# Kernel tuning notes

Hardware: AMD Instinct MI355X
Metric: run time of the kernel (lower is better)

The kernel has to match this reference:

```python
import jax, jax.numpy as jnp
import numpy as np

B, N, E, DIN, DOUT = 2, 50000, 800000, 128, 128
ALPHA = 0.2  # LeakyReLU negative slope


def setup_inputs() -> dict:
    key = jax.random.key(0)
    k1, k2, k3, k4 = jax.random.split(key, 4)
    h = jax.random.normal(k1, (B, N, DIN), dtype=jnp.float32)
    edge_index = jax.random.randint(k4, (2, E), 0, N, dtype=jnp.int32)
    # Linear(in, out, bias=False): weight shape [out, in]
    W_fc = jax.random.normal(k2, (DOUT, DIN), dtype=jnp.float32) / np.sqrt(DIN)
    # Linear(2*out, 1, bias=False): weight shape [1, 2*out]
    W_attn = jax.random.normal(k3, (1, 2 * DOUT), dtype=jnp.float32) / np.sqrt(2 * DOUT)
    return {"h": h, "edge_index": edge_index, "W_fc": W_fc, "W_attn": W_attn}


def reference(h, edge_index, W_fc, W_attn):
    # Wh: [B, N, DOUT]
    Wh = jnp.einsum("bni,oi->bno", h, W_fc)
    src, dst = edge_index[0], edge_index[1]
    # attn_fc([src_h, dst_h]) == src_h @ a_src + dst_h @ a_dst
    a = W_attn[0]
    a_src, a_dst = a[:DOUT], a[DOUT:]
    s_src = Wh @ a_src  # [B, N]
    s_dst = Wh @ a_dst  # [B, N]
    e = jax.nn.leaky_relu(s_src[:, src] + s_dst[:, dst], ALPHA)  # [B, E]
    # segment softmax over destination groups (segment ops need leading E axis)
    eT = e.T  # [E, B]
    m = jax.ops.segment_max(eT, dst, num_segments=N)  # [N, B]; -inf for empty segs (never gathered)
    ex = jnp.exp(eT - m[dst])  # [E, B]
    denom = jax.ops.segment_sum(ex, dst, num_segments=N)  # [N, B]
    attn = ex / denom[dst]  # [E, B]
    # weighted scatter-add of source features: msg [E, B, DOUT]
    msg = attn[:, :, None] * jnp.transpose(Wh, (1, 0, 2))[src]
    out = jax.ops.segment_sum(msg, dst, num_segments=N)  # [N, B, DOUT]
    return jax.nn.elu(jnp.transpose(out, (1, 0, 2)))  # [B, N, DOUT]
```

## Files before the change

### kernel.cpp

```cpp
#include <hip/hip_runtime.h>
#include <math.h>

#define NN 50000
#define EE 800000
#define DDIM 128
#define NROWS 100000
#define NBIN 391
#define NCHUNK 391
#define GEMMB 1563

typedef __attribute__((ext_vector_type(8))) short bf16x8;
typedef __attribute__((ext_vector_type(4))) float f32x4;

__device__ __forceinline__ float lrelu(float x) { return x > 0.f ? x : 0.2f * x; }
__device__ __forceinline__ float eluf(float x)  {
    float e = __expf(x);
    return x > 0.f ? x : e - 1.f;
}

__device__ __forceinline__ unsigned short f2bf(float f) {
    unsigned int u = __float_as_uint(f);
    u += 0x7fffu + ((u >> 16) & 1u);
    return (unsigned short)(u >> 16);
}
__device__ __forceinline__ float bflo(unsigned int v) { return __uint_as_float(v << 16); }
__device__ __forceinline__ float bfhi(unsigned int v) { return __uint_as_float(v & 0xffff0000u); }

__global__ __launch_bounds__(256) void wprep_kernel(const float* __restrict__ Wfc,
                                                    unsigned short* __restrict__ Wsw) {
    const int tid = threadIdx.x;
    const int col = tid & 127;
    const int kh  = tid >> 7;
#pragma unroll
    for (int q8 = 0; q8 < 8; ++q8) {
        int k0 = kh * 64 + q8 * 8;
        float4 w0 = *(const float4*)&Wfc[col * DDIM + k0];
        float4 w1 = *(const float4*)&Wfc[col * DDIM + k0 + 4];
        union { uint4 q4; unsigned short u[8]; } pk;
        pk.u[0] = f2bf(w0.x); pk.u[1] = f2bf(w0.y);
        pk.u[2] = f2bf(w0.z); pk.u[3] = f2bf(w0.w);
        pk.u[4] = f2bf(w1.x); pk.u[5] = f2bf(w1.y);
        pk.u[6] = f2bf(w1.z); pk.u[7] = f2bf(w1.w);
        int chunk = (k0 >> 3) ^ (col & 15);
        *(uint4*)((char*)Wsw + col * 256 + chunk * 16) = pk.q4;
    }
}

__global__ __launch_bounds__(256) void fused_kernel(const int* __restrict__ ei,
                                                    int* __restrict__ histmat,
                                                    const float* __restrict__ h,
                                                    const unsigned short* __restrict__ Wsw,
                                                    const float* __restrict__ Wat,
                                                    unsigned short* __restrict__ Wh16,
                                                    float* __restrict__ ssrc,
                                                    float* __restrict__ sdst) {
    __shared__ unsigned int Wlds_u32[8192];
    __shared__ unsigned short stage[64 * 136];
    const int tid = threadIdx.x;

    if (blockIdx.x < NCHUNK) {
        int* lcnt = (int*)Wlds_u32;
        for (int i = tid; i < NBIN; i += 256) lcnt[i] = 0;
        __syncthreads();
        const int cb  = blockIdx.x * 2048;
        const int cnt = min(2048, EE - cb);
#pragma unroll
        for (int r = 0; r < 8; ++r) {
            int el = r * 256 + tid;
            if (el < cnt) atomicAdd(&lcnt[ei[EE + cb + el] >> 7], 1);
        }
        __syncthreads();
        for (int i = tid; i < NBIN; i += 256)
            histmat[blockIdx.x * NBIN + i] = lcnt[i];
        return;
    }

    char* WldsB  = (char*)Wlds_u32;
    char* stageB = (char*)stage;
    const int gb   = blockIdx.x - NCHUNK;
    const int lane = tid & 63;
    const int wv   = tid >> 6;

    {
        const char* gsrc = (const char*)Wsw + wv * 8192 + lane * 16;
        unsigned int* ldst = &Wlds_u32[wv * 2048];
#pragma unroll
        for (int c8 = 0; c8 < 8; ++c8) {
            __builtin_amdgcn_global_load_lds((const unsigned int*)(gsrc + c8 * 1024),
                                             ldst + c8 * 256, 16, 0, 0);
        }
    }

    const long mbase  = (long)gb * 64 + wv * 16;
    const bool active = (mbase < NROWS);
    const long mload  = active ? mbase : 0;
    const int c  = lane & 15;
    const int kg = lane >> 4;

    union Af { bf16x8 v; unsigned short u[8]; };
    Af af[4];
    const float* arow = h + (mload + c) * DDIM + kg * 8;
#pragma unroll
    for (int kk = 0; kk < 4; ++kk) {
        float4 x = *(const float4*)(arow + kk * 32);
        float4 y = *(const float4*)(arow + kk * 32 + 4);
        af[kk].u[0] = f2bf(x.x); af[kk].u[1] = f2bf(x.y);
        af[kk].u[2] = f2bf(x.z); af[kk].u[3] = f2bf(x.w);
        af[kk].u[4] = f2bf(y.x); af[kk].u[5] = f2bf(y.y);
        af[kk].u[6] = f2bf(y.z); af[kk].u[7] = f2bf(y.w);
    }
    __syncthreads();
    if (!active) return;

    f32x4 acc[8];
#pragma unroll
    for (int t = 0; t < 8; ++t) acc[t] = (f32x4){0.f, 0.f, 0.f, 0.f};
#pragma unroll
    for (int t = 0; t < 8; ++t) {
        int colbase = (t * 16 + c) * 256;
        int sw = c << 4;
#pragma unroll
        for (int kk = 0; kk < 4; ++kk) {
            int ba = (colbase + kk * 64 + kg * 16) ^ sw;
            bf16x8 b = *(const bf16x8*)(WldsB + ba);
            acc[t] = __builtin_amdgcn_mfma_f32_16x16x32_bf16(af[kk].v, b, acc[t], 0, 0, 0);
        }
    }

#pragma unroll
    for (int t = 0; t < 8; ++t) {
#pragma unroll
        for (int r = 0; r < 4; ++r) {
            int lrow = wv * 16 + kg * 4 + r;
            *(unsigned short*)(stageB + lrow * 272 + (t * 16 + c) * 2) = f2bf(acc[t][r]);
        }
    }
    {
        const long gbase = mbase * 256;
        const int  lbase = wv * 16 * 272;
#pragma unroll
        for (int q = 0; q < 4; ++q) {
            int f = q * 1024 + lane * 16;
            uint4 v = *(const uint4*)(stageB + lbase + (f >> 8) * 272 + (f & 255));
            *(uint4*)((char*)Wh16 + gbase + f) = v;
        }
    }

    float asv[8], adv[8];
#pragma unroll
    for (int t = 0; t < 8; ++t) {
        asv[t] = Wat[t * 16 + c];
        adv[t] = Wat[DDIM + t * 16 + c];
    }
#pragma unroll
    for (int r = 0; r < 4; ++r) {
        float ps = 0.f, pd = 0.f;
#pragma unroll
        for (int t = 0; t < 8; ++t) {
            ps += acc[t][r] * asv[t];
            pd += acc[t][r] * adv[t];
        }
#pragma unroll
        for (int o = 1; o <= 8; o <<= 1) {
            ps += __shfl_xor(ps, o);
            pd += __shfl_xor(pd, o);
        }
        if (c == 0) {
            long row = mbase + kg * 4 + r;
            ssrc[row] = ps;
            sdst[row] = pd;
        }
    }
}

__global__ __launch_bounds__(64) void colscan_kernel(const int* __restrict__ histmat,
                                                     int* __restrict__ chunkstart,
                                                     int* __restrict__ bintot) {
    const int bin  = blockIdx.x;
    const int lane = threadIdx.x;
    int carry = 0;
#pragma unroll
    for (int it = 0; it < 7; ++it) {
        int c = it * 64 + lane;
        int v = (c < NCHUNK) ? histmat[c * NBIN + bin] : 0;
        int x = v;
#pragma unroll
        for (int o = 1; o < 64; o <<= 1) {
            int t = __shfl_up(x, o);
            if (lane >= o) x += t;
        }
        if (c < NCHUNK) chunkstart[bin * NCHUNK + c] = carry + x - v;
        carry += __shfl(x, 63);
    }
    if (lane == 0) bintot[bin] = carry;
}

__global__ __launch_bounds__(64) void binscan_kernel(const int* __restrict__ bintot,
                                                     int* __restrict__ binbase) {
    const int lane = threadIdx.x;
    int carry = 0;
#pragma unroll
    for (int it = 0; it < 7; ++it) {
        int c = it * 64 + lane;
        int v = (c < NBIN) ? bintot[c] : 0;
        int x = v;
#pragma unroll
        for (int o = 1; o < 64; o <<= 1) {
            int t = __shfl_up(x, o);
            if (lane >= o) x += t;
        }
        if (c < NBIN) binbase[c] = carry + x - v;
        carry += __shfl(x, 63);
    }
    if (lane == 0) binbase[NBIN] = carry;
}

__global__ __launch_bounds__(256) void scatterA_kernel(const int* __restrict__ ei,
                                                       const int* __restrict__ binbase,
                                                       const int* __restrict__ chunkstart,
                                                       unsigned int* __restrict__ records) {
    __shared__ int lcnt[NBIN];
    __shared__ int lbase[NBIN];
    const int tid = threadIdx.x;
    for (int i = tid; i < NBIN; i += 256) {
        lcnt[i]  = 0;
        lbase[i] = binbase[i] + chunkstart[i * NCHUNK + blockIdx.x];
    }
    __syncthreads();
    const int cb  = blockIdx.x * 2048;
    const int cnt = min(2048, EE - cb);
#pragma unroll
    for (int r = 0; r < 8; ++r) {
        int el = r * 256 + tid;
        if (el < cnt) {
            int e   = cb + el;
            int dst = ei[EE + e];
            int src = ei[e];
            int bin = dst >> 7;
            int rank = atomicAdd(&lcnt[bin], 1);
            records[lbase[bin] + rank] = (unsigned)src | ((unsigned)(dst & 127) << 16);
        }
    }
}

__global__ __launch_bounds__(256) void scatterB_kernel(const unsigned int* __restrict__ records,
                                                       const int* __restrict__ binbase,
                                                       int* __restrict__ offs,
                                                       int* __restrict__ slist) {
    __shared__ int cnt[128];
    __shared__ int cbase[128];
    const int b = blockIdx.x, tid = threadIdx.x;
    const int start = binbase[b];
    const int end   = binbase[b + 1];
    const int span  = end - start;

    if (tid < 128) cnt[tid] = 0;
    __syncthreads();
    for (int i = tid; i < span; i += 256)
        atomicAdd(&cnt[records[start + i] >> 16], 1);
    __syncthreads();
    if (tid < 64) {
        int l = tid;
        int c0 = cnt[l], c1 = cnt[64 + l];
        int s0 = c0, s1 = c1;
#pragma unroll
        for (int o = 1; o < 64; o <<= 1) { int t = __shfl_up(s0, o); if (l >= o) s0 += t; }
        int t0 = __shfl(s0, 63);
#pragma unroll
        for (int o = 1; o < 64; o <<= 1) { int t = __shfl_up(s1, o); if (l >= o) s1 += t; }
        cbase[l]      = s0 - c0;
        cbase[64 + l] = t0 + s1 - c1;
    }
    __syncthreads();
    if (tid < 128) {
        offs[b * 128 + tid] = start + cbase[tid];
        cnt[tid] = 0;
    }
    __syncthreads();
    for (int i = tid; i < span; i += 256) {
        unsigned int r = records[start + i];
        int dl = (int)(r >> 16);
        int pos = atomicAdd(&cnt[dl], 1);
        slist[start + cbase[dl] + pos] = (int)(r & 0xFFFFu);
    }
}

__global__ __launch_bounds__(256) void aggregate_kernel(const unsigned int* __restrict__ Wh16u,
                                                        const int* __restrict__ offs,
                                                        const int* __restrict__ slist,
                                                        const float* __restrict__ ssrc,
                                                        const float* __restrict__ sdst,
                                                        float* __restrict__ out) {
    const int lane = threadIdx.x & 63;
    const int wid  = threadIdx.x >> 6;
    const int bid  = blockIdx.x;
    const int b    = bid & 1;
    const int d    = (bid >> 1) * 4 + wid;

    const int grp = lane >> 4;
    const int fl  = lane & 15;

    float* o = out + ((long)b * NN + d) * DDIM;

    const int base   = offs[d];
    const int degree = offs[d + 1] - base;
    if (degree == 0) {
        if (lane < 16) {
            float4 z = {0.f, 0.f, 0.f, 0.f};
            ((float4*)o)[2 * fl]     = z;
            ((float4*)o)[2 * fl + 1] = z;
        }
        return;
    }

    const long boff = (long)b * NN;
    const float sdv = sdst[boff + d];
    const float* ssb = ssrc + boff;
    const unsigned int* WB = Wh16u + boff * 64;

    f32x4 accA = {0,0,0,0}, accB = {0,0,0,0};
    float ds = 0.f;

    for (int ch = 0; ch < degree; ch += 64) {
        int i = ch + lane;
        int s = 0; float w = 0.f;
        if (i < degree) {
            s = slist[base + i];
            w = __expf(lrelu(ssb[s] + sdv));
            ds += w;
        }
        int cnt   = min(64, degree - ch);
        int quads = (cnt + 3) >> 2;
        for (int j = 0; j < quads; ++j) {
            int idx = 4 * j + grp;
            int   sj = __shfl(s, idx);
            float wj = __shfl(w, idx);
            uint4 v = ((const uint4*)(WB + (long)sj * 64))[fl];
            accA.x += wj * bflo(v.x); accA.y += wj * bfhi(v.x);
            accA.z += wj * bflo(v.y); accA.w += wj * bfhi(v.y);
            accB.x += wj * bflo(v.z); accB.y += wj * bfhi(v.z);
            accB.z += wj * bflo(v.w); accB.w += wj * bfhi(v.w);
        }
    }

#pragma unroll
    for (int m = 32; m >= 16; m >>= 1) {
        accA.x += __shfl_xor(accA.x, m); accA.y += __shfl_xor(accA.y, m);
        accA.z += __shfl_xor(accA.z, m); accA.w += __shfl_xor(accA.w, m);
        accB.x += __shfl_xor(accB.x, m); accB.y += __shfl_xor(accB.y, m);
        accB.z += __shfl_xor(accB.z, m); accB.w += __shfl_xor(accB.w, m);
    }
#pragma unroll
    for (int m = 32; m > 0; m >>= 1) ds += __shfl_xor(ds, m);
    const float inv = 1.f / ds;

    if (lane < 16) {
        float4 rA = { eluf(accA.x * inv), eluf(accA.y * inv),
                      eluf(accA.z * inv), eluf(accA.w * inv) };
        float4 rB = { eluf(accB.x * inv), eluf(accB.y * inv),
                      eluf(accB.z * inv), eluf(accB.w * inv) };
        ((float4*)o)[2 * fl]     = rA;
        ((float4*)o)[2 * fl + 1] = rB;
    }
}

extern "C" void kernel_launch(void* const* d_in, const int* in_sizes, int n_in,
                              void* d_out, int out_size, void* d_ws, size_t ws_size,
                              hipStream_t stream) {
    (void)in_sizes; (void)n_in; (void)out_size; (void)ws_size;
    const float* h   = (const float*)d_in[0];
    const int*   ei  = (const int*)d_in[1];
    const float* Wfc = (const float*)d_in[2];
    const float* Wat = (const float*)d_in[3];
    float* out = (float*)d_out;

    char* ws = (char*)d_ws;
    unsigned short* Wh16 = (unsigned short*)(ws + 0);
    float*  ssrc  = (float*)(ws + 25600000);
    float*  sdst  = (float*)(ws + 26000000);
    int*    slist = (int*)  (ws + 26400000);
    unsigned int* records = (unsigned int*)(ws + 29600000);
    int*    offs      = (int*)(ws + 32800000);
    int*    histmat   = (int*)(ws + 33000192);
    int*    chunkstart= (int*)(ws + 33611716);
    int*    bintot    = (int*)(ws + 34223240);
    int*    binbase   = (int*)(ws + 34224804);
    unsigned short* Wsw = (unsigned short*)(ws + 34226384);

    wprep_kernel<<<1, 256, 0, stream>>>(Wfc, Wsw);
    fused_kernel<<<NCHUNK + GEMMB, 256, 0, stream>>>(ei, histmat, h, Wsw, Wat,
                                                     Wh16, ssrc, sdst);
    colscan_kernel<<<NBIN, 64, 0, stream>>>(histmat, chunkstart, bintot);
    binscan_kernel<<<1, 64, 0, stream>>>(bintot, binbase);
    scatterA_kernel<<<NCHUNK, 256, 0, stream>>>(ei, binbase, chunkstart, records);
    scatterB_kernel<<<NBIN, 256, 0, stream>>>(records, binbase, offs, slist);
    aggregate_kernel<<<25000, 256, 0, stream>>>((const unsigned int*)Wh16, offs,
                                                slist, ssrc, sdst, out);
}
```

Before: 116.5 us.

## Regroup pipeline stages to cut launches and hide scatter under GEMM

The destination histogram moves into the weight-prep kernel, and the scatter-to-bins pass now runs in the same grid as the feature GEMM, so the two overlap. The separate bin-scan kernel is removed: each scatter block, and each scatterB block, recomputes the 391-entry exclusive scan of bin totals locally. The launch sequence drops from seven kernels to five. In exchange every block repeats a small scan, and the binbase buffer is gone.

```diff
diff --git a/kernel.cpp b/kernel.cpp
--- a/kernel.cpp
+++ b/kernel.cpp
@@ -26,9 +26,27 @@
 __device__ __forceinline__ float bflo(unsigned int v) { return __uint_as_float(v << 16); }
 __device__ __forceinline__ float bfhi(unsigned int v) { return __uint_as_float(v & 0xffff0000u); }
 
-__global__ __launch_bounds__(256) void wprep_kernel(const float* __restrict__ Wfc,
+__global__ __launch_bounds__(256) void histW_kernel(const int* __restrict__ ei,
+                                                    int* __restrict__ histmat,
+                                                    const float* __restrict__ Wfc,
                                                     unsigned short* __restrict__ Wsw) {
     const int tid = threadIdx.x;
+    if (blockIdx.x < NCHUNK) {
+        __shared__ int lcnt[NBIN];
+        for (int i = tid; i < NBIN; i += 256) lcnt[i] = 0;
+        __syncthreads();
+        const int cb  = blockIdx.x * 2048;
+        const int cnt = min(2048, EE - cb);
+#pragma unroll
+        for (int r = 0; r < 8; ++r) {
+            int el = r * 256 + tid;
+            if (el < cnt) atomicAdd(&lcnt[ei[EE + cb + el] >> 7], 1);
+        }
+        __syncthreads();
+        for (int i = tid; i < NBIN; i += 256)
+            histmat[blockIdx.x * NBIN + i] = lcnt[i];
+        return;
+    }
     const int col = tid & 127;
     const int kh  = tid >> 7;
 #pragma unroll
@@ -46,32 +64,82 @@
     }
 }
 
-__global__ __launch_bounds__(256) void fused_kernel(const int* __restrict__ ei,
-                                                    int* __restrict__ histmat,
-                                                    const float* __restrict__ h,
-                                                    const unsigned short* __restrict__ Wsw,
-                                                    const float* __restrict__ Wat,
-                                                    unsigned short* __restrict__ Wh16,
-                                                    float* __restrict__ ssrc,
-                                                    float* __restrict__ sdst) {
+__global__ __launch_bounds__(64) void colscan_kernel(const int* __restrict__ histmat,
+                                                     int* __restrict__ chunkstart,
+                                                     int* __restrict__ bintot) {
+    const int bin  = blockIdx.x;
+    const int lane = threadIdx.x;
+    int carry = 0;
+#pragma unroll
+    for (int it = 0; it < 7; ++it) {
+        int c = it * 64 + lane;
+        int v = (c < NCHUNK) ? histmat[c * NBIN + bin] : 0;
+        int x = v;
+#pragma unroll
+        for (int o = 1; o < 64; o <<= 1) {
+            int t = __shfl_up(x, o);
+            if (lane >= o) x += t;
+        }
+        if (c < NCHUNK) chunkstart[bin * NCHUNK + c] = carry + x - v;
+        carry += __shfl(x, 63);
+    }
+    if (lane == 0) bintot[bin] = carry;
+}
+
+__global__ __launch_bounds__(256) void fusedAG_kernel(const int* __restrict__ ei,
+                                                      const int* __restrict__ bintot,
+                                                      const int* __restrict__ chunkstart,
+                                                      unsigned int* __restrict__ records,
+                                                      const float* __restrict__ h,
+                                                      const unsigned short* __restrict__ Wsw,
+                                                      const float* __restrict__ Wat,
+                                                      unsigned short* __restrict__ Wh16,
+                                                      float* __restrict__ ssrc,
+                                                      float* __restrict__ sdst) {
     __shared__ unsigned int Wlds_u32[8192];
     __shared__ unsigned short stage[64 * 136];
     const int tid = threadIdx.x;
 
     if (blockIdx.x < NCHUNK) {
-        int* lcnt = (int*)Wlds_u32;
-        for (int i = tid; i < NBIN; i += 256) lcnt[i] = 0;
+        int* lcnt  = (int*)Wlds_u32;
+        int* lbase = (int*)Wlds_u32 + 512;
+        int* bb    = (int*)Wlds_u32 + 1024;
+        if (tid < 64) {
+            int carry = 0;
+#pragma unroll
+            for (int it = 0; it < 7; ++it) {
+                int c = it * 64 + tid;
+                int v = (c < NBIN) ? bintot[c] : 0;
+                int x = v;
+#pragma unroll
+                for (int o = 1; o < 64; o <<= 1) {
+                    int t = __shfl_up(x, o);
+                    if (tid >= o) x += t;
+                }
+                if (c < NBIN) bb[c] = carry + x - v;
+                carry += __shfl(x, 63);
+            }
+        }
+        __syncthreads();
+        for (int i = tid; i < NBIN; i += 256) {
+            lcnt[i]  = 0;
+            lbase[i] = bb[i] + chunkstart[i * NCHUNK + blockIdx.x];
+        }
         __syncthreads();
         const int cb  = blockIdx.x * 2048;
         const int cnt = min(2048, EE - cb);
 #pragma unroll
         for (int r = 0; r < 8; ++r) {
             int el = r * 256 + tid;
-            if (el < cnt) atomicAdd(&lcnt[ei[EE + cb + el] >> 7], 1);
-        }
-        __syncthreads();
-        for (int i = tid; i < NBIN; i += 256)
-            histmat[blockIdx.x * NBIN + i] = lcnt[i];
+            if (el < cnt) {
+                int e   = cb + el;
+                int dst = ei[EE + e];
+                int src = ei[e];
+                int bin = dst >> 7;
+                int rank = atomicAdd(&lcnt[bin], 1);
+                records[lbase[bin] + rank] = (unsigned)src | ((unsigned)(dst & 127) << 16);
+            }
+        }
         return;
     }
 
@@ -137,11 +205,11 @@
     }
     {
         const long gbase = mbase * 256;
-        const int  lbase = wv * 16 * 272;
+        const int  lbase2 = wv * 16 * 272;
 #pragma unroll
         for (int q = 0; q < 4; ++q) {
             int f = q * 1024 + lane * 16;
-            uint4 v = *(const uint4*)(stageB + lbase + (f >> 8) * 272 + (f & 255));
+            uint4 v = *(const uint4*)(stageB + lbase2 + (f >> 8) * 272 + (f & 255));
             *(uint4*)((char*)Wh16 + gbase + f) = v;
         }
     }
@@ -173,89 +241,38 @@
     }
 }
 
-__global__ __launch_bounds__(64) void colscan_kernel(const int* __restrict__ histmat,
-                                                     int* __restrict__ chunkstart,
-                                                     int* __restrict__ bintot) {
-    const int bin  = blockIdx.x;
-    const int lane = threadIdx.x;
-    int carry = 0;
-#pragma unroll
-    for (int it = 0; it < 7; ++it) {
-        int c = it * 64 + lane;
-        int v = (c < NCHUNK) ? histmat[c * NBIN + bin] : 0;
-        int x = v;
-#pragma unroll
-        for (int o = 1; o < 64; o <<= 1) {
-            int t = __shfl_up(x, o);
-            if (lane >= o) x += t;
-        }
-        if (c < NCHUNK) chunkstart[bin * NCHUNK + c] = carry + x - v;
-        carry += __shfl(x, 63);
-    }
-    if (lane == 0) bintot[bin] = carry;
-}
-
-__global__ __launch_bounds__(64) void binscan_kernel(const int* __restrict__ bintot,
-                                                     int* __restrict__ binbase) {
-    const int lane = threadIdx.x;
-    int carry = 0;
-#pragma unroll
-    for (int it = 0; it < 7; ++it) {
-        int c = it * 64 + lane;
-        int v = (c < NBIN) ? bintot[c] : 0;
-        int x = v;
-#pragma unroll
-        for (int o = 1; o < 64; o <<= 1) {
-            int t = __shfl_up(x, o);
-            if (lane >= o) x += t;
-        }
-        if (c < NBIN) binbase[c] = carry + x - v;
-        carry += __shfl(x, 63);
-    }
-    if (lane == 0) binbase[NBIN] = carry;
-}
-
-__global__ __launch_bounds__(256) void scatterA_kernel(const int* __restrict__ ei,
-                                                       const int* __restrict__ binbase,
-                                                       const int* __restrict__ chunkstart,
-                                                       unsigned int* __restrict__ records) {
-    __shared__ int lcnt[NBIN];
-    __shared__ int lbase[NBIN];
-    const int tid = threadIdx.x;
-    for (int i = tid; i < NBIN; i += 256) {
-        lcnt[i]  = 0;
-        lbase[i] = binbase[i] + chunkstart[i * NCHUNK + blockIdx.x];
-    }
-    __syncthreads();
-    const int cb  = blockIdx.x * 2048;
-    const int cnt = min(2048, EE - cb);
-#pragma unroll
-    for (int r = 0; r < 8; ++r) {
-        int el = r * 256 + tid;
-        if (el < cnt) {
-            int e   = cb + el;
-            int dst = ei[EE + e];
-            int src = ei[e];
-            int bin = dst >> 7;
-            int rank = atomicAdd(&lcnt[bin], 1);
-            records[lbase[bin] + rank] = (unsigned)src | ((unsigned)(dst & 127) << 16);
-        }
-    }
-}
-
 __global__ __launch_bounds__(256) void scatterB_kernel(const unsigned int* __restrict__ records,
-                                                       const int* __restrict__ binbase,
+                                                       const int* __restrict__ bintot,
                                                        int* __restrict__ offs,
                                                        int* __restrict__ slist) {
     __shared__ int cnt[128];
     __shared__ int cbase[128];
+    __shared__ int bb2[2];
     const int b = blockIdx.x, tid = threadIdx.x;
-    const int start = binbase[b];
-    const int end   = binbase[b + 1];
-    const int span  = end - start;
-
+
+    if (tid < 64) {
+        int carry = 0;
+#pragma unroll
+        for (int it = 0; it < 7; ++it) {
+            int c = it * 64 + tid;
+            int v = (c < NBIN) ? bintot[c] : 0;
+            int x = v;
+#pragma unroll
+            for (int o = 1; o < 64; o <<= 1) {
+                int t = __shfl_up(x, o);
+                if (tid >= o) x += t;
+            }
+            int excl = carry + x - v;
+            if (c == b)     bb2[0] = excl;
+            if (c == b + 1) bb2[1] = excl;
+            carry += __shfl(x, 63);
+        }
+    }
     if (tid < 128) cnt[tid] = 0;
     __syncthreads();
+    const int start = bb2[0];
+    const int span  = bb2[1] - start;
+
     for (int i = tid; i < span; i += 256)
         atomicAdd(&cnt[records[start + i] >> 16], 1);
     __syncthreads();
@@ -384,16 +401,13 @@
     int*    histmat   = (int*)(ws + 33000192);
     int*    chunkstart= (int*)(ws + 33611716);
     int*    bintot    = (int*)(ws + 34223240);
-    int*    binbase   = (int*)(ws + 34224804);
-    unsigned short* Wsw = (unsigned short*)(ws + 34226384);
-
-    wprep_kernel<<<1, 256, 0, stream>>>(Wfc, Wsw);
-    fused_kernel<<<NCHUNK + GEMMB, 256, 0, stream>>>(ei, histmat, h, Wsw, Wat,
-                                                     Wh16, ssrc, sdst);
+    unsigned short* Wsw = (unsigned short*)(ws + 34224816);
+
+    histW_kernel<<<NCHUNK + 1, 256, 0, stream>>>(ei, histmat, Wfc, Wsw);
     colscan_kernel<<<NBIN, 64, 0, stream>>>(histmat, chunkstart, bintot);
-    binscan_kernel<<<1, 64, 0, stream>>>(bintot, binbase);
-    scatterA_kernel<<<NCHUNK, 256, 0, stream>>>(ei, binbase, chunkstart, records);
-    scatterB_kernel<<<NBIN, 256, 0, stream>>>(records, binbase, offs, slist);
+    fusedAG_kernel<<<NCHUNK + GEMMB, 256, 0, stream>>>(ei, bintot, chunkstart, records,
+                                                       h, Wsw, Wat, Wh16, ssrc, sdst);
+    scatterB_kernel<<<NBIN, 256, 0, stream>>>(records, bintot, offs, slist);
     aggregate_kernel<<<25000, 256, 0, stream>>>((const unsigned int*)Wh16, offs,
                                                 slist, ssrc, sdst, out);
 }
```

Result: faster. 111.9 us (-4.0%).
